# Kernel tuning notes

Measured on AMD Instinct MI355X. Metric: run time of the kernel, lower is better.

The kernel has to match this reference:

```python
import jax, jax.numpy as jnp
import numpy as np

NUM_CARDS = 40
NUM_SUITS = 4
SIDE_SUIT_LEN = 9
NUM_ACTIONS = 2 * NUM_CARDS + 1  # 81 (use_signals=True)
NUM_TRICKS = 10


def setup_inputs() -> dict:
    key = jax.random.key(0)
    ks = jax.random.split(key, 8)
    B, A, D_in, D_q = 16384, 40, 4096, 256
    backbone_embed = jax.random.normal(ks[0], (B, D_in), dtype=jnp.float32)
    rank = jax.random.randint(ks[1], (B, A), -1, SIDE_SUIT_LEN)
    # guarantee at least one valid action per row (slot 0)
    rank = rank.at[:, 0].set(jnp.maximum(rank[:, 0], 0))
    suit = jax.random.randint(ks[2], (B, A), 0, NUM_SUITS + 1)  # suit==NUM_SUITS -> no-signal action
    valid_actions = jnp.stack([rank, suit], axis=-1)
    phase = jax.random.randint(ks[3], (B,), 0, 2)
    trick = jax.random.randint(ks[4], (B,), 0, NUM_TRICKS)
    # params
    Wq = jax.random.normal(ks[5], (D_in, D_q), dtype=jnp.float32) / np.sqrt(D_in).astype(np.float32)
    bq = jnp.zeros((D_q,), jnp.float32)
    key_table = jax.random.normal(ks[6], (NUM_ACTIONS, D_q), dtype=jnp.float32)
    ln_gamma = jnp.ones((D_q,), jnp.float32)
    ln_beta = jnp.zeros((D_q,), jnp.float32)
    # signal_prior == 'lin': p_signal = 2 / (num_tricks_left + 1)
    num_left = NUM_TRICKS - jnp.arange(NUM_TRICKS, dtype=jnp.float32)
    p_signal = 2.0 / (num_left + 1.0)
    return dict(backbone_embed=backbone_embed, valid_actions=valid_actions, phase=phase,
                trick=trick, Wq=Wq, bq=bq, key_table=key_table, ln_gamma=ln_gamma,
                ln_beta=ln_beta, p_signal=p_signal)


def reference(backbone_embed, valid_actions, phase, trick, Wq, bq, key_table, ln_gamma, ln_beta, p_signal):
    D_q = Wq.shape[1]
    rank = valid_actions[..., 0]          # (B, A)
    suit = valid_actions[..., 1]          # (B, A)
    aidx = phase[:, None] * NUM_CARDS + suit * SIDE_SUIT_LEN + rank
    aidx = jnp.where(rank == -1, -1, jnp.where(suit == NUM_SUITS, 2 * NUM_CARDS, aidx))
    # PaddedEmbed: shift by 1, row 0 is the zero padding row for idx == -1
    table = jnp.concatenate([jnp.zeros((1, D_q), key_table.dtype), key_table], axis=0)
    k = table[aidx + 1]                   # (B, A, D_q)
    # LayerNorm over last dim
    mu = k.mean(axis=-1, keepdims=True)
    var = k.var(axis=-1, keepdims=True)
    k = (k - mu) * jax.lax.rsqrt(var + 1e-5) * ln_gamma + ln_beta
    q = backbone_embed @ Wq + bq          # (B, D_q)
    attn = jnp.einsum('bq,baq->ba', q, k) / jnp.sqrt(jnp.float32(D_q))
    attn = jnp.where(rank == -1, -jnp.inf, attn)
    # no-signal bias on action 0 during signal phase
    n_valid = (rank != -1).sum(axis=-1).astype(jnp.float32)
    ps = p_signal[trick]
    w = jnp.log(jnp.maximum((1.0 - ps) / ps * (n_valid - 1.0), 1e-5))
    w = jnp.where(n_valid == 1.0, 0.0, w)
    attn = attn.at[:, 0].add(jnp.where(phase == 1, w, 0.0))
    return jax.nn.log_softmax(attn, axis=-1)
```

## Files before the change

kernel.cpp:

```cpp
#include <hip/hip_runtime.h>
#include <hip/hip_bf16.h>
#include <math.h>


typedef _Float16 half8_t __attribute__((ext_vector_type(8)));
typedef float    f32x4_t __attribute__((ext_vector_type(4)));

#define NUM_B 16384
#define D_IN  4096
#define D_Q   256
#define N_ACT 40

__device__ __forceinline__ half8_t cvt8(const float4 a, const float4 b) {
  half8_t h;
  h[0] = (_Float16)a.x; h[1] = (_Float16)a.y; h[2] = (_Float16)a.z; h[3] = (_Float16)a.w;
  h[4] = (_Float16)b.x; h[5] = (_Float16)b.y; h[6] = (_Float16)b.z; h[7] = (_Float16)b.w;
  return h;
}
__device__ __forceinline__ void gl_lds16f(const float* g, float* l) {
  __builtin_amdgcn_global_load_lds(
      (const __attribute__((address_space(1))) void*)g,
      (__attribute__((address_space(3))) void*)l, 16, 0, 0);
}
__device__ __forceinline__ void gl_lds16h(const _Float16* g, _Float16* l) {
  __builtin_amdgcn_global_load_lds(
      (const __attribute__((address_space(1))) void*)g,
      (__attribute__((address_space(3))) void*)l, 16, 0, 0);
}

__global__ __launch_bounds__(256) void ln_table_k(const float* __restrict__ kt,
                                                  const float* __restrict__ gamma,
                                                  const float* __restrict__ beta,
                                                  const float* __restrict__ bq,
                                                  float* __restrict__ out,
                                                  float* __restrict__ bqk) {
  __shared__ float red[8];
  __shared__ float red2[4];
  const int t = threadIdx.x, r = blockIdx.x;
  float v = kt[r * 256 + t];
  float s = v, sq = v * v;
#pragma unroll
  for (int off = 1; off < 64; off <<= 1) {
    s  += __shfl_xor(s, off);
    sq += __shfl_xor(sq, off);
  }
  if ((t & 63) == 0) { red[t >> 6] = s; red[4 + (t >> 6)] = sq; }
  __syncthreads();
  s  = red[0] + red[1] + red[2] + red[3];
  sq = red[4] + red[5] + red[6] + red[7];
  const float mu  = s * (1.0f / 256.0f);
  const float var = sq * (1.0f / 256.0f) - mu * mu;
  const float inv = 1.0f / sqrtf(var + 1e-5f);
  const float o = (v - mu) * inv * gamma[t] + beta[t];
  out[r * 256 + t] = o;
  float p = o * bq[t];
#pragma unroll
  for (int off = 1; off < 64; off <<= 1) p += __shfl_xor(p, off);
  if ((t & 63) == 0) red2[t >> 6] = p;
  __syncthreads();
  if (t == 0) bqk[r] = red2[0] + red2[1] + red2[2] + red2[3];
}

__global__ __launch_bounds__(256) void wk_gemm_k(const float* __restrict__ Wq,
                                                 const float* __restrict__ tbl,
                                                 _Float16* __restrict__ Bf) {
  const int lane = threadIdx.x & 63, w = threadIdx.x >> 6;
  const int wm = w >> 1, wn = w & 1;
  const int m0 = blockIdx.x * 64 + wm * 32;
  const int n0 = wn * 64;
  const int fr = lane & 15, fg = lane >> 4;
  f32x4_t acc[2][4] = {};
  for (int k0 = 0; k0 < 256; k0 += 32) {
    half8_t af[2], bf[4];
#pragma unroll
    for (int i = 0; i < 2; ++i) {
      const float* p = Wq + (size_t)(m0 + i * 16 + fr) * D_Q + k0 + fg * 8;
      af[i] = cvt8(*(const float4*)p, *(const float4*)(p + 4));
    }
#pragma unroll
    for (int j = 0; j < 4; ++j) {
      const int n = n0 + j * 16 + fr;
      if (n < 81) {
        const float* p = tbl + (size_t)n * D_Q + k0 + fg * 8;
        bf[j] = cvt8(*(const float4*)p, *(const float4*)(p + 4));
      } else {
        bf[j] = (half8_t)(_Float16)0.0f;
      }
    }
#pragma unroll
    for (int i = 0; i < 2; ++i)
#pragma unroll
      for (int j = 0; j < 4; ++j)
        acc[i][j] = __builtin_amdgcn_mfma_f32_16x16x32_f16(af[i], bf[j], acc[i][j], 0, 0, 0);
  }
#pragma unroll
  for (int i = 0; i < 2; ++i)
#pragma unroll
    for (int j = 0; j < 4; ++j)
#pragma unroll
      for (int r = 0; r < 4; ++r) {
        const int k = m0 + i * 16 + fg * 4 + r;
        const int n = n0 + j * 16 + fr;
        const int kt32 = k >> 5, fgb = (k >> 3) & 3, e = k & 7;
        const int jg = n >> 4, frb = n & 15;
        Bf[(((size_t)kt32 * 8 + jg) * 64 + fgb * 16 + frb) * 8 + e] =
            (_Float16)acc[i][j][r];
      }
}

__global__ __launch_bounds__(256, 4) void gemm_part_k(const float* __restrict__ A,
                                                      const _Float16* __restrict__ Bf,
                                                      float* __restrict__ part) {
  __shared__ __align__(16) char smem[32768];
  float*    Afs = (float*)smem;
  _Float16* Bls = (_Float16*)(smem + 16384);

  const int t = threadIdx.x, lane = t & 63, w = t >> 6;
  const int fr = lane & 15, fg = lane >> 4;
  const int ks = blockIdx.y;
  const size_t row0 = (size_t)blockIdx.x * 64;
  const int k0 = ks * 1024;

#define STAGE(T)                                                              \
  do {                                                                        \
    _Pragma("unroll") for (int q_ = 0; q_ < 8; ++q_) {                        \
      const int id_ = w * 8 + q_;                                             \
      if (id_ < 16) {                                                         \
        const int r_ = id_ * 4 + (lane >> 4);                                 \
        gl_lds16f(A + (size_t)(row0 + r_) * D_IN + k0 + (T)*64 +              \
                      (((lane & 15) ^ (r_ & 7)) << 2),                        \
                  Afs + id_ * 256);                                           \
      } else {                                                                \
        const int ib_ = id_ - 16;                                             \
        gl_lds16h(Bf + ((size_t)(ks * 16 + (T))) * 8192 + ib_ * 512 + lane * 8, \
                  Bls + ib_ * 512);                                           \
      }                                                                       \
    }                                                                         \
  } while (0)

  const int wm = w >> 1, wn = w & 1;
  int aoff[2][2][2];
#pragma unroll
  for (int i = 0; i < 2; ++i)
#pragma unroll
    for (int c = 0; c < 2; ++c)
#pragma unroll
      for (int h = 0; h < 2; ++h) {
        const int R = wm * 32 + i * 16 + fr;
        aoff[i][c][h] = R * 64 + (((c * 8 + fg * 2 + h) ^ (R & 7)) << 2);
      }
  int boff[2][4];
#pragma unroll
  for (int c = 0; c < 2; ++c)
#pragma unroll
    for (int j = 0; j < 4; ++j)
      boff[c][j] = c * 4096 + (wn * 4 + j) * 512 + lane * 8;

  f32x4_t acc[2][4] = {};

  STAGE(0);
  __syncthreads();
  for (int kt = 0; kt < 16; ++kt) {
#pragma unroll
    for (int c = 0; c < 2; ++c) {
      half8_t bfv[4];
#pragma unroll
      for (int j = 0; j < 4; ++j) bfv[j] = *(const half8_t*)(Bls + boff[c][j]);
#pragma unroll
      for (int i = 0; i < 2; ++i) {
        const float4 x0 = *(const float4*)(Afs + aoff[i][c][0]);
        const float4 x1 = *(const float4*)(Afs + aoff[i][c][1]);
        const half8_t af = cvt8(x0, x1);
#pragma unroll
        for (int j = 0; j < 4; ++j)
          acc[i][j] = __builtin_amdgcn_mfma_f32_16x16x32_f16(af, bfv[j], acc[i][j], 0, 0, 0);
      }
    }
    if (kt < 15) {
      __syncthreads();
      STAGE(kt + 1);
      __syncthreads();
    }
  }
#undef STAGE

  float* pb = part + ((size_t)ks * NUM_B + row0) * 128;
#pragma unroll
  for (int i = 0; i < 2; ++i)
#pragma unroll
    for (int j = 0; j < 4; ++j) {
      const int col = wn * 64 + j * 16 + fr;
#pragma unroll
      for (int r = 0; r < 4; ++r)
        pb[(size_t)(wm * 32 + i * 16 + fg * 4 + r) * 128 + col] = acc[i][j][r];
    }
}

__global__ __launch_bounds__(256) void softmax_k(const float* __restrict__ part,
                                                 const float* __restrict__ bqk,
                                                 const int* __restrict__ va,
                                                 const int* __restrict__ phase,
                                                 const int* __restrict__ trick,
                                                 const float* __restrict__ psig,
                                                 float* __restrict__ out) {
  const int t = threadIdx.x;
  const int lane = t & 63, w = t >> 6;
  const int b = blockIdx.x * 4 + w;

  float sx = 0.f, sy = 0.f;
#pragma unroll
  for (int ks = 0; ks < 4; ++ks) {
    const float2 v = *(const float2*)&part[((size_t)ks * NUM_B + b) * 128 + lane * 2];
    sx += v.x; sy += v.y;
  }

  int rank = -1, suit = 0;
  if (lane < N_ACT) {
    rank = va[((size_t)b * N_ACT + lane) * 2];
    suit = va[((size_t)b * N_ACT + lane) * 2 + 1];
  }
  const int ph = phase[b];
  const bool valid = (rank >= 0);
  const int aidx = valid ? (suit == 4 ? 80 : ph * 40 + suit * 9 + rank) : -1;
  const int nvalid = __popcll(__ballot(valid));

  const int srcl = valid ? (aidx >> 1) : 0;
  const float v0 = __shfl(sx, srcl);
  const float v1 = __shfl(sy, srcl);

  float attn_l = -INFINITY;
  if (valid) attn_l = (((aidx & 1) ? v1 : v0) + bqk[aidx]) * 0.0625f;

  if (ph == 1 && lane == 0) {
    const float ps = psig[trick[b]];
    const float nv = (float)nvalid;
    const float wv = (nv == 1.0f) ? 0.0f
                                  : logf(fmaxf((1.0f - ps) / ps * (nv - 1.0f), 1e-5f));
    attn_l += wv;
  }

  float m = attn_l;
#pragma unroll
  for (int off = 1; off < 64; off <<= 1) m = fmaxf(m, __shfl_xor(m, off));
  const float e = expf(attn_l - m);
  float ssum = e;
#pragma unroll
  for (int off = 1; off < 64; off <<= 1) ssum += __shfl_xor(ssum, off);
  const float o = attn_l - m - logf(ssum);
  if (lane < N_ACT) out[(size_t)b * N_ACT + lane] = valid ? o : -3.0e38f;
}

extern "C" void kernel_launch(void* const* d_in, const int* in_sizes, int n_in,
                              void* d_out, int out_size, void* d_ws, size_t ws_size,
                              hipStream_t stream) {
  const float* backbone = (const float*)d_in[0];
  const int*   va       = (const int*)d_in[1];
  const int*   phase    = (const int*)d_in[2];
  const int*   trick    = (const int*)d_in[3];
  const float* Wq       = (const float*)d_in[4];
  const float* bq       = (const float*)d_in[5];
  const float* keytab   = (const float*)d_in[6];
  const float* gamma    = (const float*)d_in[7];
  const float* beta     = (const float*)d_in[8];
  const float* psig     = (const float*)d_in[9];
  float* out = (float*)d_out;

  char* ws = (char*)d_ws;
  _Float16* Bf   = (_Float16*)ws;
  float* tableLN = (float*)(ws + (1u << 20));
  float* bqk     = (float*)(ws + (1u << 20) + (128u << 10));
  float* part    = (float*)(ws + (2u << 20));

  ln_table_k<<<dim3(81), 256, 0, stream>>>(keytab, gamma, beta, bq, tableLN, bqk);
  wk_gemm_k<<<dim3(64), 256, 0, stream>>>(Wq, tableLN, Bf);
  gemm_part_k<<<dim3(NUM_B / 64, 4), 256, 0, stream>>>(backbone, Bf, part);
  softmax_k<<<dim3(NUM_B / 4), 256, 0, stream>>>(part, bqk, va, phase, trick,
                                                 psig, out);
}
```

Before: 103.6 us.

## Double-buffer GEMM LDS with register-staged fp16 A tile and larger blocks

The main GEMM kernel now uses 512 threads covering 128 rows per block. A is loaded into registers, converted to fp16 once, and written to LDS, where it was previously copied as fp32 via global_load_lds and converted on every read. A and B are double-buffered in LDS, so the loads for the next k-step are issued before the MFMA loop of the current step, cutting one barrier per iteration. This targets load latency and repeated conversion cost, but doubles LDS use to 64KB and adds register pressure, which may reduce occupancy.

```diff
diff --git a/kernel.cpp b/kernel.cpp
--- a/kernel.cpp
+++ b/kernel.cpp
@@ -4,6 +4,7 @@
 
 
 typedef _Float16 half8_t __attribute__((ext_vector_type(8)));
+typedef _Float16 half4_t __attribute__((ext_vector_type(4)));
 typedef float    f32x4_t __attribute__((ext_vector_type(4)));
 
 #define NUM_B 16384
@@ -17,10 +18,10 @@
   h[4] = (_Float16)b.x; h[5] = (_Float16)b.y; h[6] = (_Float16)b.z; h[7] = (_Float16)b.w;
   return h;
 }
-__device__ __forceinline__ void gl_lds16f(const float* g, float* l) {
-  __builtin_amdgcn_global_load_lds(
-      (const __attribute__((address_space(1))) void*)g,
-      (__attribute__((address_space(3))) void*)l, 16, 0, 0);
+__device__ __forceinline__ half4_t cvt4(const float4 a) {
+  half4_t h;
+  h[0] = (_Float16)a.x; h[1] = (_Float16)a.y; h[2] = (_Float16)a.z; h[3] = (_Float16)a.w;
+  return h;
 }
 __device__ __forceinline__ void gl_lds16h(const _Float16* g, _Float16* l) {
   __builtin_amdgcn_global_load_lds(
@@ -108,47 +109,56 @@
       }
 }
 
-__global__ __launch_bounds__(256, 4) void gemm_part_k(const float* __restrict__ A,
+__global__ __launch_bounds__(512, 4) void gemm_part_k(const float* __restrict__ A,
                                                       const _Float16* __restrict__ Bf,
                                                       float* __restrict__ part) {
-  __shared__ __align__(16) char smem[32768];
-  float*    Afs = (float*)smem;
-  _Float16* Bls = (_Float16*)(smem + 16384);
+  __shared__ __align__(16) char smem[65536];
+  _Float16* Als = (_Float16*)smem;
+  _Float16* Bls = (_Float16*)(smem + 32768);
 
   const int t = threadIdx.x, lane = t & 63, w = t >> 6;
   const int fr = lane & 15, fg = lane >> 4;
   const int ks = blockIdx.y;
-  const size_t row0 = (size_t)blockIdx.x * 64;
+  const size_t row0 = (size_t)blockIdx.x * 128;
   const int k0 = ks * 1024;
 
-#define STAGE(T)                                                              \
+  const int arow[4] = {w * 16 + 0 * 4 + (lane >> 4), w * 16 + 1 * 4 + (lane >> 4),
+                       w * 16 + 2 * 4 + (lane >> 4), w * 16 + 3 * 4 + (lane >> 4)};
+  const float* abase = A + k0 + (lane & 15) * 4;
+  int awo[4];
+#pragma unroll
+  for (int q = 0; q < 4; ++q)
+    awo[q] = arow[q] * 64 + ((((lane & 15) >> 1) ^ (arow[q] & 7)) * 8) + (lane & 1) * 4;
+
+#define ISSUE_A(T)                                                            \
   do {                                                                        \
-    _Pragma("unroll") for (int q_ = 0; q_ < 8; ++q_) {                        \
-      const int id_ = w * 8 + q_;                                             \
-      if (id_ < 16) {                                                         \
-        const int r_ = id_ * 4 + (lane >> 4);                                 \
-        gl_lds16f(A + (size_t)(row0 + r_) * D_IN + k0 + (T)*64 +              \
-                      (((lane & 15) ^ (r_ & 7)) << 2),                        \
-                  Afs + id_ * 256);                                           \
-      } else {                                                                \
-        const int ib_ = id_ - 16;                                             \
-        gl_lds16h(Bf + ((size_t)(ks * 16 + (T))) * 8192 + ib_ * 512 + lane * 8, \
-                  Bls + ib_ * 512);                                           \
-      }                                                                       \
+    _Pragma("unroll") for (int q_ = 0; q_ < 4; ++q_)                          \
+        ar[q_] = *(const float4*)(abase + (size_t)(row0 + arow[q_]) * D_IN +  \
+                                  (T)*64);                                    \
+  } while (0)
+#define STAGE_B(T, P)                                                         \
+  do {                                                                        \
+    _Pragma("unroll") for (int q_ = 0; q_ < 2; ++q_) {                        \
+      const int ib_ = w * 2 + q_;                                             \
+      gl_lds16h(Bf + ((size_t)(ks * 16 + (T))) * 8192 + ib_ * 512 + lane * 8, \
+                Bls + (P)*8192 + ib_ * 512);                                  \
     }                                                                         \
   } while (0)
+#define WRITE_A(P)                                                            \
+  do {                                                                        \
+    _Pragma("unroll") for (int q_ = 0; q_ < 4; ++q_)                          \
+        *(half4_t*)(Als + (P)*8192 + awo[q_]) = cvt4(ar[q_]);                 \
+  } while (0)
 
   const int wm = w >> 1, wn = w & 1;
-  int aoff[2][2][2];
+  int aoff[2][2];
 #pragma unroll
   for (int i = 0; i < 2; ++i)
 #pragma unroll
-    for (int c = 0; c < 2; ++c)
-#pragma unroll
-      for (int h = 0; h < 2; ++h) {
-        const int R = wm * 32 + i * 16 + fr;
-        aoff[i][c][h] = R * 64 + (((c * 8 + fg * 2 + h) ^ (R & 7)) << 2);
-      }
+    for (int c = 0; c < 2; ++c) {
+      const int R = wm * 32 + i * 16 + fr;
+      aoff[i][c] = R * 64 + (((c * 4 + fg) ^ (R & 7)) * 8);
+    }
   int boff[2][4];
 #pragma unroll
   for (int c = 0; c < 2; ++c)
@@ -157,32 +167,53 @@
       boff[c][j] = c * 4096 + (wn * 4 + j) * 512 + lane * 8;
 
   f32x4_t acc[2][4] = {};
-
-  STAGE(0);
-  __syncthreads();
+  float4 ar[4];
+
+  STAGE_B(0, 0);
+  ISSUE_A(0);
+  __builtin_amdgcn_sched_barrier(0);
+  asm volatile("s_waitcnt vmcnt(0)" ::: "memory");
+  WRITE_A(0);
+  asm volatile("s_waitcnt lgkmcnt(0)" ::: "memory");
+  __builtin_amdgcn_s_barrier();
+  __builtin_amdgcn_sched_barrier(0);
+
   for (int kt = 0; kt < 16; ++kt) {
+    const int p = kt & 1;
+    if (kt < 15) {
+      STAGE_B(kt + 1, p ^ 1);
+      ISSUE_A(kt + 1);
+    }
+    __builtin_amdgcn_sched_barrier(0);
+
+    const _Float16* Ap = Als + p * 8192;
+    const _Float16* Bp = Bls + p * 8192;
 #pragma unroll
     for (int c = 0; c < 2; ++c) {
       half8_t bfv[4];
 #pragma unroll
-      for (int j = 0; j < 4; ++j) bfv[j] = *(const half8_t*)(Bls + boff[c][j]);
+      for (int j = 0; j < 4; ++j) bfv[j] = *(const half8_t*)(Bp + boff[c][j]);
 #pragma unroll
       for (int i = 0; i < 2; ++i) {
-        const float4 x0 = *(const float4*)(Afs + aoff[i][c][0]);
-        const float4 x1 = *(const float4*)(Afs + aoff[i][c][1]);
-        const half8_t af = cvt8(x0, x1);
+        const half8_t af = *(const half8_t*)(Ap + aoff[i][c]);
 #pragma unroll
         for (int j = 0; j < 4; ++j)
           acc[i][j] = __builtin_amdgcn_mfma_f32_16x16x32_f16(af, bfv[j], acc[i][j], 0, 0, 0);
       }
     }
+    __builtin_amdgcn_sched_barrier(0);
+
     if (kt < 15) {
-      __syncthreads();
-      STAGE(kt + 1);
-      __syncthreads();
-    }
-  }
-#undef STAGE
+      asm volatile("s_waitcnt vmcnt(0)" ::: "memory");
+      WRITE_A(p ^ 1);
+      asm volatile("s_waitcnt lgkmcnt(0)" ::: "memory");
+      __builtin_amdgcn_s_barrier();
+      __builtin_amdgcn_sched_barrier(0);
+    }
+  }
+#undef ISSUE_A
+#undef STAGE_B
+#undef WRITE_A
 
   float* pb = part + ((size_t)ks * NUM_B + row0) * 128;
 #pragma unroll
@@ -273,7 +304,7 @@
 
   ln_table_k<<<dim3(81), 256, 0, stream>>>(keytab, gamma, beta, bq, tableLN, bqk);
   wk_gemm_k<<<dim3(64), 256, 0, stream>>>(Wq, tableLN, Bf);
-  gemm_part_k<<<dim3(NUM_B / 64, 4), 256, 0, stream>>>(backbone, Bf, part);
+  gemm_part_k<<<dim3(NUM_B / 128, 4), 512, 0, stream>>>(backbone, Bf, part);
   softmax_k<<<dim3(NUM_B / 4), 256, 0, stream>>>(part, bqk, va, phase, trick,
                                                  psig, out);
 }
```

Measured after the change: 106.7 us. 3.0% more time.
